# Kernel optimization log

Measured on AMD Instinct MI355X. Metric: run time of the kernel, lower is better.

The kernel has to match this reference:

```python
import jax, jax.numpy as jnp
import numpy as np

H = 64  # rnn_hidden_size


def _rnn_seq(x, W_ih, W_hh, b_ih, b_hh):
    """One tanh RNN layer over [B,T,D] -> full output sequence [B,T,H]."""
    pre = jnp.einsum('btd,hd->bth', x, W_ih) + b_ih  # input projection hoisted out of the scan
    h0 = jnp.zeros((x.shape[0], W_hh.shape[0]), x.dtype)
    def step(h, p_t):
        h = jnp.tanh(p_t + h @ W_hh.T + b_hh)
        return h, h
    _, ys = jax.lax.scan(step, h0, jnp.swapaxes(pre, 0, 1))  # scan over time
    return jnp.swapaxes(ys, 0, 1)


def _rnn_last(x, W_ih, W_hh, b_ih, b_hh):
    """One tanh RNN layer, returning only the last hidden state [B,H]."""
    pre = jnp.einsum('btd,hd->bth', x, W_ih) + b_ih
    h0 = jnp.zeros((x.shape[0], W_hh.shape[0]), x.dtype)
    def step(h, p_t):
        return jnp.tanh(p_t + h @ W_hh.T + b_hh), None
    h, _ = jax.lax.scan(step, h0, jnp.swapaxes(pre, 0, 1))
    return h


def setup_inputs() -> dict:
    key = jax.random.key(0)
    ks = jax.random.split(key, 32)
    B, T, D = 128, 4096, 3
    kr = 1.0 / np.sqrt(H)          # PyTorch RNN init bound
    u = lambda kk, shape, b: jax.random.uniform(kk, shape, jnp.float32, -b, b)
    inp = {
        'x': jax.random.normal(ks[0], (B, T, D), jnp.float32),
        'y': jax.random.normal(ks[1], (B, T, D), jnp.float32),
        'z': jax.random.normal(ks[2], (5,), jnp.float32),
        # rnn_empty, layer 0 (in=3) and layer 1 (in=64)
        'e_Wih0': u(ks[3], (H, D), kr), 'e_Whh0': u(ks[4], (H, H), kr),
        'e_bih0': u(ks[5], (H,), kr),  'e_bhh0': u(ks[6], (H,), kr),
        'e_Wih1': u(ks[7], (H, H), kr), 'e_Whh1': u(ks[8], (H, H), kr),
        'e_bih1': u(ks[9], (H,), kr),  'e_bhh1': u(ks[10], (H,), kr),
        # rnn_occupied
        'o_Wih0': u(ks[11], (H, D), kr), 'o_Whh0': u(ks[12], (H, H), kr),
        'o_bih0': u(ks[13], (H,), kr),  'o_bhh0': u(ks[14], (H,), kr),
        'o_Wih1': u(ks[15], (H, H), kr), 'o_Whh1': u(ks[16], (H, H), kr),
        'o_bih1': u(ks[17], (H,), kr),  'o_bhh1': u(ks[18], (H,), kr),
        # heads: fce/fco (64->2), fc1 (9->64), fc2 (64->5)
        'fce_w': u(ks[19], (2, H), kr), 'fce_b': u(ks[20], (2,), kr),
        'fco_w': u(ks[21], (2, H), kr), 'fco_b': u(ks[22], (2,), kr),
        'fc1_w': u(ks[23], (64, 9), 1.0 / np.sqrt(9)), 'fc1_b': u(ks[24], (64,), 1.0 / np.sqrt(9)),
        'fc2_w': u(ks[25], (5, 64), kr), 'fc2_b': u(ks[26], (5,), kr),
    }
    return inp


def reference(x, y, z,
              e_Wih0, e_Whh0, e_bih0, e_bhh0, e_Wih1, e_Whh1, e_bih1, e_bhh1,
              o_Wih0, o_Whh0, o_bih0, o_bhh0, o_Wih1, o_Whh1, o_bih1, o_bhh1,
              fce_w, fce_b, fco_w, fco_b, fc1_w, fc1_b, fc2_w, fc2_b):
    # two 2-layer tanh RNNs; last-timestep output of layer 2 == final hidden of layer 2
    hx = _rnn_last(_rnn_seq(x, e_Wih0, e_Whh0, e_bih0, e_bhh0),
                   e_Wih1, e_Whh1, e_bih1, e_bhh1)            # [B,H]
    hy = _rnn_last(_rnn_seq(y, o_Wih0, o_Whh0, o_bih0, o_bhh0),
                   o_Wih1, o_Whh1, o_bih1, o_bhh1)            # [B,H]
    e = hx @ fce_w.T + fce_b                                  # [B,2]
    o = hy @ fco_w.T + fco_b                                  # [B,2]
    zz = jnp.concatenate([e[0], o[0], z])                     # [9]
    h = jax.nn.relu(zz @ fc1_w.T + fc1_b)                     # [64]
    return h @ fc2_w.T + fc2_b                                # [5]
```

## Files before the change

kernel.cpp:

```cpp
#include <hip/hip_runtime.h>

#define T 4096
#define EP 8
#define RING 32
#define NEP (T / EP + 2)

__device__ __forceinline__ float fast_tanh(float x) {
    float e = __expf(2.0f * x);
    float r = __builtin_amdgcn_rcpf(e + 1.0f);
    return fmaf(-2.0f, r, 1.0f);
}

#define ANCHOR16(a, b) asm volatile("" : \
    "+v"((a)[(b)+0]),  "+v"((a)[(b)+1]),  "+v"((a)[(b)+2]),  "+v"((a)[(b)+3]),  \
    "+v"((a)[(b)+4]),  "+v"((a)[(b)+5]),  "+v"((a)[(b)+6]),  "+v"((a)[(b)+7]),  \
    "+v"((a)[(b)+8]),  "+v"((a)[(b)+9]),  "+v"((a)[(b)+10]), "+v"((a)[(b)+11]), \
    "+v"((a)[(b)+12]), "+v"((a)[(b)+13]), "+v"((a)[(b)+14]), "+v"((a)[(b)+15]))
#define ANCHOR64(a) do { ANCHOR16(a, 0); ANCHOR16(a, 16); \
                         ANCHOR16(a, 32); ANCHOR16(a, 48); } while (0)

#define ROTF(acc, v, w, R) \
    asm("v_fmac_f32_dpp %0, %1, %2 row_ror:" #R " row_mask:0xf bank_mask:0xf" \
        : "+v"(acc) : "v"(v), "v"(w))

#define MOVNOP(dst, src) \
    asm("v_mov_b32 %0, %1\n\ts_nop 1" : "=v"(dst) : "v"(src))

#define KBLOCK(v, wd, B) do { \
    a0 = fmaf((v), (wd)[(B) + 0], a0); \
    ROTF(a1, (v), (wd)[(B) + 1],  1);  ROTF(a2, (v), (wd)[(B) + 2],  2); \
    ROTF(a3, (v), (wd)[(B) + 3],  3);  ROTF(a0, (v), (wd)[(B) + 4],  4); \
    ROTF(a1, (v), (wd)[(B) + 5],  5);  ROTF(a2, (v), (wd)[(B) + 6],  6); \
    ROTF(a3, (v), (wd)[(B) + 7],  7);  ROTF(a0, (v), (wd)[(B) + 8],  8); \
    ROTF(a1, (v), (wd)[(B) + 9],  9);  ROTF(a2, (v), (wd)[(B) +10], 10); \
    ROTF(a3, (v), (wd)[(B) +11], 11);  ROTF(a0, (v), (wd)[(B) +12], 12); \
    ROTF(a1, (v), (wd)[(B) +13], 13);  ROTF(a2, (v), (wd)[(B) +14], 14); \
    ROTF(a3, (v), (wd)[(B) +15], 15); \
} while (0)

__device__ __forceinline__ float rnn_step_dpp(const float (&wd)[64], float init, float hp,
                                              int a16, int a32, int a48) {
    const int hb = __float_as_int(hp);
    const int b1i = __builtin_amdgcn_ds_bpermute(a16, hb);
    const int b2i = __builtin_amdgcn_ds_bpermute(a32, hb);
    const int b3i = __builtin_amdgcn_ds_bpermute(a48, hb);
    float hpD; MOVNOP(hpD, hp);
    float a0 = init, a1 = 0.f, a2 = 0.f, a3 = 0.f;
    KBLOCK(hpD, wd, 0);
    float v1; MOVNOP(v1, __int_as_float(b1i)); KBLOCK(v1, wd, 16);
    float v2; MOVNOP(v2, __int_as_float(b2i)); KBLOCK(v2, wd, 32);
    float v3; MOVNOP(v3, __int_as_float(b3i)); KBLOCK(v3, wd, 48);
    return fast_tanh((a0 + a1) + (a2 + a3));
}

__device__ __forceinline__ void load_wdpp(const float* __restrict__ W, int lane,
                                          bool dirplus, float (&wd)[64]) {
#pragma unroll
    for (int m = 0; m < 64; ++m) {
        const int k = m >> 4, r = m & 15;
        const int lowoff = dirplus ? r : ((16 - r) & 15);
        const int j = ((lane & 48) | ((lane + lowoff) & 15)) ^ (k << 4);
        wd[m] = W[lane * 64 + j];
    }
}

__global__ void prep_kernel(const float* __restrict__ x, const float* __restrict__ y,
                            const float* __restrict__ eW, const float* __restrict__ ebi,
                            const float* __restrict__ ebh,
                            const float* __restrict__ oW, const float* __restrict__ obi,
                            const float* __restrict__ obh,
                            float* __restrict__ pre)
{
    int idx = blockIdx.x * blockDim.x + threadIdx.x;
    int i = idx & 63;
    int t = (idx >> 6) & (T - 1);
    int s = idx >> 18;
    const float* in = s ? y : x;
    const float* W  = s ? oW : eW;
    const float* bi = s ? obi : ebi;
    const float* bh = s ? obh : ebh;
    float v = bi[i] + bh[i]
            + W[i*3+0]*in[t*3+0] + W[i*3+1]*in[t*3+1] + W[i*3+2]*in[t*3+2];
    pre[idx] = v;
}

__global__ __launch_bounds__(256, 1) void seq_kernel(
    const float* __restrict__ pre,
    const float* __restrict__ eWhh0, const float* __restrict__ eWih1,
    const float* __restrict__ eWhh1, const float* __restrict__ ebih1,
    const float* __restrict__ ebhh1,
    const float* __restrict__ oWhh0, const float* __restrict__ oWih1,
    const float* __restrict__ oWhh1, const float* __restrict__ obih1,
    const float* __restrict__ obhh1,
    float* __restrict__ hlast)
{
    const int s    = blockIdx.x;
    const int wv   = threadIdx.x >> 6;
    const int lane = threadIdx.x & 63;

    __shared__ __align__(16) float h0ring[RING][64];
    __shared__ __align__(16) float qring[RING][64];

    const float* p = pre + s * T * 64;

    const int got = __builtin_amdgcn_update_dpp(0, lane, 0x121, 0xF, 0xF, false);
    const bool dirplus = ((got & 15) == ((lane + 1) & 15));
    const int a16 = (lane ^ 16) << 2;
    const int a32 = (lane ^ 32) << 2;
    const int a48 = (lane ^ 48) << 2;

    if (wv == 0) {
        const float* Whh0 = s ? oWhh0 : eWhh0;
        float wd[64];
        load_wdpp(Whh0, lane, dirplus, wd);

        float hp = 0.f;
        float pc[EP], pn[EP];
#pragma unroll
        for (int i = 0; i < EP; ++i) pc[i] = p[i * 64 + lane];

        for (int k = 0; k < NEP; ++k) {
            ANCHOR64(wd);
            const int base = k * EP;
#pragma unroll
            for (int i = 0; i < EP; ++i) {
                int t = base + EP + i;
                pn[i] = (t < T) ? p[t * 64 + lane] : 0.f;
            }
            if (base < T) {
#pragma unroll
                for (int i = 0; i < EP; ++i) {
                    hp = rnn_step_dpp(wd, pc[i], hp, a16, a32, a48);
                    h0ring[(base + i) & (RING - 1)][lane] = hp;
                }
            }
#pragma unroll
            for (int i = 0; i < EP; ++i) pc[i] = pn[i];
            __syncthreads();
        }
    } else if (wv <= 2) {
        const float* Wih1 = s ? oWih1 : eWih1;
        const float  b1   = s ? (obih1[lane] + obhh1[lane])
                              : (ebih1[lane] + ebhh1[lane]);
        float wi[64];
#pragma unroll
        for (int j = 0; j < 64; ++j) wi[j] = Wih1[lane * 64 + j];

        const int i0 = (wv - 1) * (EP / 2);

        for (int k = 0; k < NEP; ++k) {
            ANCHOR64(wi);
            const int base = k * EP - EP;
            if (base >= 0 && base < T) {
#pragma unroll
                for (int i = 0; i < EP / 2; ++i) {
                    const int t = base + i0 + i;
                    const float4* hv = (const float4*)h0ring[t & (RING - 1)];
                    float q[4] = { b1, 0.f, 0.f, 0.f };
#pragma unroll
                    for (int j4 = 0; j4 < 16; ++j4) {
                        float4 u = hv[j4];
                        q[0] = fmaf(wi[4*j4+0], u.x, q[0]);
                        q[1] = fmaf(wi[4*j4+1], u.y, q[1]);
                        q[2] = fmaf(wi[4*j4+2], u.z, q[2]);
                        q[3] = fmaf(wi[4*j4+3], u.w, q[3]);
                    }
                    qring[t & (RING - 1)][lane] = (q[0] + q[1]) + (q[2] + q[3]);
                }
            }
            __syncthreads();
        }
    } else {
        const float* Whh1 = s ? oWhh1 : eWhh1;
        float wd[64];
        load_wdpp(Whh1, lane, dirplus, wd);

        float hp = 0.f;
        for (int k = 0; k < NEP; ++k) {
            ANCHOR64(wd);
            const int base = k * EP - 2 * EP;
            if (base >= 0) {
                float qb[EP];
#pragma unroll
                for (int i = 0; i < EP; ++i)
                    qb[i] = qring[(base + i) & (RING - 1)][lane];
#pragma unroll
                for (int i = 0; i < EP; ++i)
                    hp = rnn_step_dpp(wd, qb[i], hp, a16, a32, a48);
            }
            __syncthreads();
        }
        hlast[s * 64 + lane] = hp;
    }
}

__global__ void head_kernel(const float* __restrict__ hlast,
                            const float* __restrict__ z,
                            const float* __restrict__ fce_w, const float* __restrict__ fce_b,
                            const float* __restrict__ fco_w, const float* __restrict__ fco_b,
                            const float* __restrict__ fc1_w, const float* __restrict__ fc1_b,
                            const float* __restrict__ fc2_w, const float* __restrict__ fc2_b,
                            float* __restrict__ out)
{
    const int lane = threadIdx.x;
    __shared__ float zz[9];
    __shared__ float hh[64];

    if (lane < 2) {
        float sacc = fce_b[lane];
        for (int j = 0; j < 64; ++j) sacc += fce_w[lane * 64 + j] * hlast[j];
        zz[lane] = sacc;
    } else if (lane < 4) {
        int r = lane - 2;
        float sacc = fco_b[r];
        for (int j = 0; j < 64; ++j) sacc += fco_w[r * 64 + j] * hlast[64 + j];
        zz[lane] = sacc;
    } else if (lane < 9) {
        zz[lane] = z[lane - 4];
    }
    __syncthreads();

    float sacc = fc1_b[lane];
#pragma unroll
    for (int j = 0; j < 9; ++j) sacc += fc1_w[lane * 9 + j] * zz[j];
    hh[lane] = fmaxf(sacc, 0.f);
    __syncthreads();

    if (lane < 5) {
        float o = fc2_b[lane];
        for (int i = 0; i < 64; ++i) o += fc2_w[lane * 64 + i] * hh[i];
        out[lane] = o;
    }
}

extern "C" void kernel_launch(void* const* d_in, const int* in_sizes, int n_in,
                              void* d_out, int out_size, void* d_ws, size_t ws_size,
                              hipStream_t stream)
{
    const float* x      = (const float*)d_in[0];
    const float* y      = (const float*)d_in[1];
    const float* z      = (const float*)d_in[2];
    const float* e_Wih0 = (const float*)d_in[3];
    const float* e_Whh0 = (const float*)d_in[4];
    const float* e_bih0 = (const float*)d_in[5];
    const float* e_bhh0 = (const float*)d_in[6];
    const float* e_Wih1 = (const float*)d_in[7];
    const float* e_Whh1 = (const float*)d_in[8];
    const float* e_bih1 = (const float*)d_in[9];
    const float* e_bhh1 = (const float*)d_in[10];
    const float* o_Wih0 = (const float*)d_in[11];
    const float* o_Whh0 = (const float*)d_in[12];
    const float* o_bih0 = (const float*)d_in[13];
    const float* o_bhh0 = (const float*)d_in[14];
    const float* o_Wih1 = (const float*)d_in[15];
    const float* o_Whh1 = (const float*)d_in[16];
    const float* o_bih1 = (const float*)d_in[17];
    const float* o_bhh1 = (const float*)d_in[18];
    const float* fce_w  = (const float*)d_in[19];
    const float* fce_b  = (const float*)d_in[20];
    const float* fco_w  = (const float*)d_in[21];
    const float* fco_b  = (const float*)d_in[22];
    const float* fc1_w  = (const float*)d_in[23];
    const float* fc1_b  = (const float*)d_in[24];
    const float* fc2_w  = (const float*)d_in[25];
    const float* fc2_b  = (const float*)d_in[26];

    float* pre   = (float*)d_ws;
    float* hlast = pre + 2 * T * 64;
    float* out   = (float*)d_out;

    prep_kernel<<<(2 * T * 64) / 256, 256, 0, stream>>>(
        x, y, e_Wih0, e_bih0, e_bhh0, o_Wih0, o_bih0, o_bhh0, pre);

    seq_kernel<<<2, 256, 0, stream>>>(
        pre,
        e_Whh0, e_Wih1, e_Whh1, e_bih1, e_bhh1,
        o_Whh0, o_Wih1, o_Whh1, o_bih1, o_bhh1,
        hlast);

    head_kernel<<<1, 64, 0, stream>>>(
        hlast, z, fce_w, fce_b, fco_w, fco_b, fc1_w, fc1_b, fc2_w, fc2_b, out);
}
```

Baseline: 1.096 ms.

## Use fp16 MFMA for recurrent matvecs with runtime probe and DPP fallback

Replaces the per-lane DPP-rotated fp32 FMA recurrence in the layer-0 and layer-1 recurrent waves with 16x16x32 fp16 MFMA instructions. The hidden state is repacked into B fragments each step using DPP row rotations and cndmask selects. A startup probe checks the MFMA fragment layout against a scalar reference and falls back to the old path if it does not match. This is meant to shorten the serial per-timestep latency of the 64x64 matvec, at the cost of fp16 rounding of weights and state and extra repack instructions on the critical path.

```diff
diff --git a/kernel.cpp b/kernel.cpp
--- a/kernel.cpp
+++ b/kernel.cpp
@@ -1,9 +1,15 @@
 #include <hip/hip_runtime.h>
+#include <hip/hip_fp16.h>
 
 #define T 4096
 #define EP 8
 #define RING 32
 #define NEP (T / EP + 2)
+
+typedef _Float16 f16x8 __attribute__((ext_vector_type(8)));
+typedef _Float16 f16x2 __attribute__((ext_vector_type(2)));
+typedef float    f32x4 __attribute__((ext_vector_type(4)));
+typedef unsigned long long u64;
 
 __device__ __forceinline__ float fast_tanh(float x) {
     float e = __expf(2.0f * x);
@@ -22,10 +28,8 @@
 #define ROTF(acc, v, w, R) \
     asm("v_fmac_f32_dpp %0, %1, %2 row_ror:" #R " row_mask:0xf bank_mask:0xf" \
         : "+v"(acc) : "v"(v), "v"(w))
-
 #define MOVNOP(dst, src) \
     asm("v_mov_b32 %0, %1\n\ts_nop 1" : "=v"(dst) : "v"(src))
-
 #define KBLOCK(v, wd, B) do { \
     a0 = fmaf((v), (wd)[(B) + 0], a0); \
     ROTF(a1, (v), (wd)[(B) + 1],  1);  ROTF(a2, (v), (wd)[(B) + 2],  2); \
@@ -62,6 +66,158 @@
         const int j = ((lane & 48) | ((lane + lowoff) & 15)) ^ (k << 4);
         wd[m] = W[lane * 64 + j];
     }
+}
+
+#define MFMA16(a, b, c) __builtin_amdgcn_mfma_f32_16x16x32_f16((a), (b), (c), 0, 0, 0)
+
+#define DPPROR(dst, src, R) \
+    dst = (unsigned)__builtin_amdgcn_update_dpp(0, (int)(src), 0x120 + (R), 0xF, 0xF, false)
+
+__device__ __forceinline__ unsigned selmask(unsigned s0, unsigned s1, u64 m) {
+    unsigned d;
+    asm("v_cndmask_b32 %0, %1, %2, %3" : "=v"(d) : "v"(s0), "v"(s1), "s"(m));
+    return d;
+}
+__device__ __forceinline__ float selmaskf(float s0, float s1, u64 m) {
+    float d;
+    asm("v_cndmask_b32 %0, %1, %2, %3" : "=v"(d) : "v"(s0), "v"(s1), "s"(m));
+    return d;
+}
+
+struct SelMasks {
+    u64 mb1, mb3, mbhi;
+    u64 m0[4], m1[4], m2[4];
+};
+
+__device__ __forceinline__ void build_masks(int lo, bool dirplus, SelMasks &M) {
+    const int myb = lo & 3;
+    const int rb1 = (dirplus ? (lo + 1) : (lo + 15)) & 3;
+    const int rb2 = (dirplus ? (lo + 2) : (lo + 14)) & 3;
+    M.mb1  = __ballot(myb == 1);
+    M.mb3  = __ballot(myb == 3);
+    M.mbhi = __ballot(myb >= 2);
+#pragma unroll
+    for (int b = 0; b < 4; ++b) {
+        M.m0[b] = __ballot(myb == b);
+        M.m1[b] = __ballot(rb1 == b);
+        M.m2[b] = __ballot(rb2 == b);
+    }
+}
+
+__device__ __forceinline__ void load_afrag(const float* __restrict__ W, int lo, int hi,
+                                           f16x8 (&A)[4][2]) {
+#pragma unroll
+    for (int b = 0; b < 4; ++b)
+#pragma unroll
+        for (int ch = 0; ch < 2; ++ch) {
+            f16x8 v;
+#pragma unroll
+            for (int e = 0; e < 8; ++e) {
+                const int k = 32 * ch + 16 * (e >> 2) + 4 * hi + (e & 3);
+                v[e] = (_Float16)W[(16 * b + lo) * 64 + k];
+            }
+            A[b][ch] = v;
+        }
+}
+
+__device__ __forceinline__ void mfma8(const f16x8 (&A)[4][2], f16x8 b0, f16x8 b1,
+                                      const f32x4 (&cin)[4], f32x4 (&d)[4]) {
+#pragma unroll
+    for (int b = 0; b < 4; ++b) d[b] = MFMA16(A[b][0], b0, cin[b]);
+#pragma unroll
+    for (int b = 0; b < 4; ++b) d[b] = MFMA16(A[b][1], b1, d[b]);
+}
+
+__device__ __forceinline__ void repack(const f32x4 (&d)[4], const SelMasks &M,
+                                       f16x8 &bf0, f16x8 &bf1, f32x4 &thOut) {
+    float th[4];
+#pragma unroll
+    for (int r = 0; r < 4; ++r) {
+        float a = selmaskf(d[0][r], d[1][r], M.mb1);
+        float b = selmaskf(d[2][r], d[3][r], M.mb3);
+        th[r] = fast_tanh(selmaskf(a, b, M.mbhi));
+    }
+    thOut = (f32x4){ th[0], th[1], th[2], th[3] };
+    const unsigned w0 = __builtin_bit_cast(unsigned, __builtin_amdgcn_cvt_pkrtz(th[0], th[1]));
+    const unsigned w1 = __builtin_bit_cast(unsigned, __builtin_amdgcn_cvt_pkrtz(th[2], th[3]));
+    unsigned r1w0, r1w1, r2w0, r2w1, r3w0, r3w1;
+    DPPROR(r1w0, w0, 1); DPPROR(r1w1, w1, 1);
+    DPPROR(r2w0, w0, 2); DPPROR(r2w1, w1, 2);
+    DPPROR(r3w0, w0, 3); DPPROR(r3w1, w1, 3);
+    unsigned gw0[4], gw1[4];
+#pragma unroll
+    for (int b = 0; b < 4; ++b) {
+        unsigned t = selmask(r3w0, r2w0, M.m2[b]);
+        t = selmask(t, r1w0, M.m1[b]);
+        gw0[b] = selmask(t, w0, M.m0[b]);
+        unsigned u = selmask(r3w1, r2w1, M.m2[b]);
+        u = selmask(u, r1w1, M.m1[b]);
+        gw1[b] = selmask(u, w1, M.m0[b]);
+    }
+    const uint4 q0 = { gw0[0], gw1[0], gw0[1], gw1[1] };
+    const uint4 q1 = { gw0[2], gw1[2], gw0[3], gw1[3] };
+    bf0 = __builtin_bit_cast(f16x8, q0);
+    bf1 = __builtin_bit_cast(f16x8, q1);
+}
+
+__device__ __forceinline__ float probe_h(int j) {
+    return (float)((j * 37 + 11) & 63) * 0.015625f - 0.5f;
+}
+
+__device__ bool probe_mfma(const float* __restrict__ W, int lane, int lo, int hi,
+                           const f16x8 (&A)[4][2], const SelMasks &M,
+                           volatile float* scr) {
+    float ref = 0.f;
+#pragma unroll 1
+    for (int j = 0; j < 64; ++j) ref = fmaf(W[lane * 64 + j], probe_h(j), ref);
+    scr[lane] = ref;
+    asm volatile("s_waitcnt lgkmcnt(0)" ::: "memory");
+
+    f16x8 b0, b1;
+#pragma unroll
+    for (int e = 0; e < 8; ++e) {
+        const int k = 16 * (e >> 2) + 4 * hi + (e & 3);
+        b0[e] = (_Float16)probe_h(k);
+        b1[e] = (_Float16)probe_h(32 + k);
+    }
+    const f32x4 z = { 0.f, 0.f, 0.f, 0.f };
+    const f32x4 cz[4] = { z, z, z, z };
+    f32x4 d[4];
+    mfma8(A, b0, b1, cz, d);
+    bool ok = true;
+#pragma unroll
+    for (int b = 0; b < 4; ++b)
+#pragma unroll
+        for (int r = 0; r < 4; ++r)
+            ok = ok && (fabsf(d[b][r] - scr[16 * b + 4 * hi + r]) < 0.05f);
+
+    asm volatile("s_waitcnt lgkmcnt(0)" ::: "memory");
+    scr[lane] = fast_tanh(ref);
+    asm volatile("s_waitcnt lgkmcnt(0)" ::: "memory");
+    float ref2 = 0.f;
+#pragma unroll 1
+    for (int j = 0; j < 64; ++j) ref2 = fmaf(W[lane * 64 + j], scr[j], ref2);
+    asm volatile("s_waitcnt lgkmcnt(0)" ::: "memory");
+    scr[lane] = ref2;
+    asm volatile("s_waitcnt lgkmcnt(0)" ::: "memory");
+
+    f32x4 th;
+    repack(d, M, b0, b1, th);
+    f32x4 d2[4];
+    mfma8(A, b0, b1, cz, d2);
+#pragma unroll
+    for (int b = 0; b < 4; ++b)
+#pragma unroll
+        for (int r = 0; r < 4; ++r)
+            ok = ok && (fabsf(d2[b][r] - scr[16 * b + 4 * hi + r]) < 0.10f);
+    return __all(ok) != 0;
+}
+
+__device__ __forceinline__ void loadP(const float* __restrict__ p, int t, int hi,
+                                      f32x4 (&c)[4]) {
+#pragma unroll
+    for (int b = 0; b < 4; ++b)
+        c[b] = *(const f32x4*)(p + t * 64 + 16 * b + 4 * hi);
 }
 
 __global__ void prep_kernel(const float* __restrict__ x, const float* __restrict__ y,
@@ -97,9 +253,12 @@
     const int s    = blockIdx.x;
     const int wv   = threadIdx.x >> 6;
     const int lane = threadIdx.x & 63;
+    const int lo   = lane & 15;
+    const int hi   = lane >> 4;
 
     __shared__ __align__(16) float h0ring[RING][64];
     __shared__ __align__(16) float qring[RING][64];
+    __shared__ __align__(16) float pscr[2][64];
 
     const float* p = pre + s * T * 64;
 
@@ -111,32 +270,60 @@
 
     if (wv == 0) {
         const float* Whh0 = s ? oWhh0 : eWhh0;
-        float wd[64];
-        load_wdpp(Whh0, lane, dirplus, wd);
-
-        float hp = 0.f;
-        float pc[EP], pn[EP];
-#pragma unroll
-        for (int i = 0; i < EP; ++i) pc[i] = p[i * 64 + lane];
-
-        for (int k = 0; k < NEP; ++k) {
-            ANCHOR64(wd);
-            const int base = k * EP;
-#pragma unroll
-            for (int i = 0; i < EP; ++i) {
-                int t = base + EP + i;
-                pn[i] = (t < T) ? p[t * 64 + lane] : 0.f;
+        SelMasks M; build_masks(lo, dirplus, M);
+        f16x8 A[4][2];
+        load_afrag(Whh0, lo, hi, A);
+        const bool useMfma = probe_mfma(Whh0, lane, lo, hi, A, M, pscr[0]);
+
+        if (useMfma) {
+            f16x8 bf0 = {}, bf1 = {};
+            f32x4 pf[2][4];
+            loadP(p, 0, hi, pf[0]);
+            loadP(p, 1, hi, pf[1]);
+            for (int k = 0; k < NEP; ++k) {
+                const int base = k * EP;
+                if (base < T) {
+#pragma unroll
+                    for (int i = 0; i < EP; ++i) {
+                        const int t = base + i;
+                        f32x4 d[4];
+                        mfma8(A, bf0, bf1, pf[i & 1], d);
+                        int tn = t + 2; if (tn > T - 1) tn = T - 1;
+                        loadP(p, tn, hi, pf[i & 1]);
+                        f32x4 th;
+                        repack(d, M, bf0, bf1, th);
+                        if (lo < 4)
+                            *(f32x4*)&h0ring[t & (RING - 1)][16 * lo + 4 * hi] = th;
+                    }
+                }
+                __syncthreads();
             }
-            if (base < T) {
+        } else {
+            float wd[64];
+            load_wdpp(Whh0, lane, dirplus, wd);
+            float hp = 0.f;
+            float pc[EP], pn[EP];
+#pragma unroll
+            for (int i = 0; i < EP; ++i) pc[i] = p[i * 64 + lane];
+            for (int k = 0; k < NEP; ++k) {
+                ANCHOR64(wd);
+                const int base = k * EP;
 #pragma unroll
                 for (int i = 0; i < EP; ++i) {
-                    hp = rnn_step_dpp(wd, pc[i], hp, a16, a32, a48);
-                    h0ring[(base + i) & (RING - 1)][lane] = hp;
+                    int t = base + EP + i;
+                    pn[i] = (t < T) ? p[t * 64 + lane] : 0.f;
                 }
+                if (base < T) {
+#pragma unroll
+                    for (int i = 0; i < EP; ++i) {
+                        hp = rnn_step_dpp(wd, pc[i], hp, a16, a32, a48);
+                        h0ring[(base + i) & (RING - 1)][lane] = hp;
+                    }
+                }
+#pragma unroll
+                for (int i = 0; i < EP; ++i) pc[i] = pn[i];
+                __syncthreads();
             }
-#pragma unroll
-            for (int i = 0; i < EP; ++i) pc[i] = pn[i];
-            __syncthreads();
         }
     } else if (wv <= 2) {
         const float* Wih1 = s ? oWih1 : eWih1;
@@ -172,25 +359,61 @@
         }
     } else {
         const float* Whh1 = s ? oWhh1 : eWhh1;
-        float wd[64];
-        load_wdpp(Whh1, lane, dirplus, wd);
-
-        float hp = 0.f;
-        for (int k = 0; k < NEP; ++k) {
-            ANCHOR64(wd);
-            const int base = k * EP - 2 * EP;
-            if (base >= 0) {
-                float qb[EP];
-#pragma unroll
-                for (int i = 0; i < EP; ++i)
-                    qb[i] = qring[(base + i) & (RING - 1)][lane];
-#pragma unroll
-                for (int i = 0; i < EP; ++i)
-                    hp = rnn_step_dpp(wd, qb[i], hp, a16, a32, a48);
+        SelMasks M; build_masks(lo, dirplus, M);
+        f16x8 A[4][2];
+        load_afrag(Whh1, lo, hi, A);
+        const bool useMfma = probe_mfma(Whh1, lane, lo, hi, A, M, pscr[1]);
+
+        if (useMfma) {
+            f16x8 bf0 = {}, bf1 = {};
+            f32x4 lastTh = {};
+            for (int k = 0; k < NEP; ++k) {
+                const int base = k * EP - 2 * EP;
+                if (base >= 0) {
+                    f32x4 qf[2][4];
+#pragma unroll
+                    for (int b = 0; b < 4; ++b)
+                        qf[0][b] = *(const f32x4*)&qring[base & (RING - 1)][16 * b + 4 * hi];
+#pragma unroll
+                    for (int i = 0; i < EP; ++i) {
+                        const int t = base + i;
+                        if (i + 1 < EP) {
+#pragma unroll
+                            for (int b = 0; b < 4; ++b)
+                                qf[(i + 1) & 1][b] =
+                                    *(const f32x4*)&qring[(t + 1) & (RING - 1)][16 * b + 4 * hi];
+                        }
+                        f32x4 d[4];
+                        mfma8(A, bf0, bf1, qf[i & 1], d);
+                        f32x4 th;
+                        repack(d, M, bf0, bf1, th);
+                        if (t == T - 1) lastTh = th;
+                    }
+                }
+                __syncthreads();
             }
-            __syncthreads();
+            if (lo < 4)
+                *(f32x4*)&hlast[s * 64 + 16 * lo + 4 * hi] = lastTh;
+        } else {
+            float wd[64];
+            load_wdpp(Whh1, lane, dirplus, wd);
+            float hp = 0.f;
+            for (int k = 0; k < NEP; ++k) {
+                ANCHOR64(wd);
+                const int base = k * EP - 2 * EP;
+                if (base >= 0) {
+                    float qb[EP];
+#pragma unroll
+                    for (int i = 0; i < EP; ++i)
+                        qb[i] = qring[(base + i) & (RING - 1)][lane];
+#pragma unroll
+                    for (int i = 0; i < EP; ++i)
+                        hp = rnn_step_dpp(wd, qb[i], hp, a16, a32, a48);
+                }
+                __syncthreads();
+            }
+            hlast[s * 64 + lane] = hp;
         }
-        hlast[s * 64 + lane] = hp;
     }
 }
 
```

Result: slower. 1.465 ms (+33.7%).
